# Kernel optimization log

Hardware: AMD Instinct MI355X
Metric: run time of the kernel (lower is better)

The kernel has to match this reference:

```python
import jax, jax.numpy as jnp
import numpy as np

B, T, I, Hd = 64, 512, 256, 512
SIGMA = 0.01


def setup_inputs() -> dict:
    key = jax.random.key(0)
    ks = jax.random.split(key, 32)
    d = {}
    d["tt_inputs"] = jax.random.normal(ks[0], (B, T, I), dtype=jnp.float32)
    d["mark_inputs"] = jax.random.normal(ks[1], (B, T, I), dtype=jnp.float32)
    i = 2
    for nm in ["W_xz_t", "W_xr_t", "W_xz_m", "W_xr_m", "W_xh"]:
        d[nm] = SIGMA * jax.random.normal(ks[i], (I, Hd), dtype=jnp.float32); i += 1
    for nm in ["W_hz_t", "W_hr_t", "W_hz_m", "W_hr_m", "W_hh"]:
        d[nm] = SIGMA * jax.random.normal(ks[i], (Hd, Hd), dtype=jnp.float32); i += 1
    for nm in ["b_z_t", "b_r_t", "b_z_m", "b_r_m", "b_h"]:
        d[nm] = jnp.zeros((Hd,), dtype=jnp.float32)
    for nm in ["fus_W_rt", "fus_W_rm", "fus_W_zt", "fus_W_zm"]:
        d[nm] = jax.random.uniform(ks[i], (Hd, Hd), minval=-0.1, maxval=0.1, dtype=jnp.float32); i += 1
    for nm in ["fus_W_xt", "fus_W_xm"]:
        d[nm] = jax.random.uniform(ks[i], (I, I), minval=-0.1, maxval=0.1, dtype=jnp.float32); i += 1
    for nm, dim in [("fus_rbias", Hd), ("fus_zbias", Hd), ("fus_xbias", I)]:
        d[nm] = jax.random.uniform(ks[i], (dim,), minval=-0.1, maxval=0.1, dtype=jnp.float32); i += 1
    return d


def reference(tt_inputs, mark_inputs,
              W_xz_t, W_xr_t, W_xz_m, W_xr_m, W_xh,
              W_hz_t, W_hr_t, W_hz_m, W_hr_m, W_hh,
              b_z_t, b_r_t, b_z_m, b_r_m, b_h,
              fus_W_rt, fus_W_rm, fus_W_zt, fus_W_zm,
              fus_W_xt, fus_W_xm,
              fus_rbias, fus_zbias, fus_xbias):
    sig = jax.nn.sigmoid
    H0 = jnp.zeros((tt_inputs.shape[0], W_hh.shape[0]), dtype=tt_inputs.dtype)

    def step(H, xs):
        X_t, X_m = xs  # each [B, I]
        Z_t = sig(X_t @ W_xz_t + H @ W_hz_t + b_z_t)
        R_t = sig(X_t @ W_xr_t + H @ W_hr_t + b_r_t)
        Z_m = sig(X_m @ W_xz_m + H @ W_hz_m + b_z_m)
        R_m = sig(X_m @ W_xr_m + H @ W_hr_m + b_r_m)
        z = sig(Z_t @ fus_W_zt + Z_m @ fus_W_zm + fus_zbias)
        Z = z * Z_t + (1 - z) * Z_m
        r = sig(R_t @ fus_W_rt + R_m @ fus_W_rm + fus_rbias)
        R = r * R_t + (1 - r) * R_m
        x = sig(X_t @ fus_W_xt + X_m @ fus_W_xm + fus_xbias)
        X = x * X_t + (1 - x) * X_m
        H_tilde = jnp.tanh(X @ W_xh + (R * H) @ W_hh + b_h)
        H_new = Z * H + (1 - Z) * H_tilde
        return H_new, H_new

    xs = (jnp.swapaxes(tt_inputs, 0, 1), jnp.swapaxes(mark_inputs, 0, 1))  # [T,B,I]
    H_last, outs = jax.lax.scan(step, H0, xs)
    outputs = jnp.swapaxes(outs, 0, 1)  # [B, T, Hd]; dropout p=0.0 -> identity
    return outputs, H_last
```

## Files before the change

kernel.cpp:

```cpp
#include <hip/hip_runtime.h>

#define DEV __device__ __forceinline__

constexpr int Bb = 64, Tt = 512, Ii = 256, Hd = 512;
constexpr int NWG = 512, NTHR = 256;
constexpr int BbHd = Bb * Hd, BbIi = Bb * Ii;


constexpr int OFF_G  = 16384;
constexpr int OFF_F  = OFF_G + 4 * BbHd;
constexpr int OFF_HB = OFF_F + 2 * BbHd;
constexpr int OFF_XB = OFF_HB + 2 * BbHd;
constexpr int OFF_AH = OFF_XB + 2 * BbIi;

#define SMEM_BYTES 32768

struct P {
  const float *tt, *mark;
  const float *Wxz_t, *Wxr_t, *Wxz_m, *Wxr_m, *Wxh;
  const float *Whz_t, *Whr_t, *Whz_m, *Whr_m, *Whh;
  const float *bz_t, *br_t, *bz_m, *br_m, *bh;
  const float *fWrt, *fWrm, *fWzt, *fWzm, *fWxt, *fWxm;
  const float *frb, *fzb, *fxb;
  float* out; float* ws;
};

enum { JA = 0, JB = 1, JRH = 2, JX = 3, JXB = 4 };

DEV float sig1(float x) { return 1.f / (1.f + __expf(-x)); }
DEV float tanh1(float x) { return 2.f * sig1(2.f * x) - 1.f; }
DEV float4 ld4(const float* p) { return *(const float4*)p; }

DEV float2 ld2v(const float* p) {
  unsigned long long u = __hip_atomic_load((const unsigned long long*)p,
                                           __ATOMIC_RELAXED, __HIP_MEMORY_SCOPE_AGENT);
  return __builtin_bit_cast(float2, u);
}
DEV void st2v(float* p, float2 v) {
  __hip_atomic_store((unsigned long long*)p, __builtin_bit_cast(unsigned long long, v),
                     __ATOMIC_RELAXED, __HIP_MEMORY_SCOPE_AGENT);
}
DEV float4 ld4v(const float* p) {
  float2 a = ld2v(p), b = ld2v(p + 2);
  return make_float4(a.x, a.y, b.x, b.y);
}

template<int TYPE>
DEV float4 loadA4(const P& p, int t, const float* aux, int side, int b, int k) {
  const float* ws = p.ws;
  if constexpr (TYPE == JA) {
    if (k < Ii) return ld4(&aux[(b * Tt + (t - 1)) * Ii + k]);
    return ld4v(ws + OFF_HB + ((t - 1) & 1) * BbHd + b * Hd + (k - Ii));
  } else if constexpr (TYPE == JB) {
    const int g = (k < Hd) ? side : side + 2;
    const int j = (k < Hd) ? k : k - Hd;
    return ld4v(ws + OFF_G + g * BbHd + b * Hd + j);
  } else if constexpr (TYPE == JRH) {
    return ld4v(ws + OFF_F + BbHd + b * Hd + k);
  } else if constexpr (TYPE == JX) {
    if (k < Ii) return ld4(&p.tt[(b * Tt + t) * Ii + k]);
    return ld4(&p.mark[(b * Tt + t) * Ii + (k - Ii)]);
  } else {
    return ld4v(ws + OFF_XB + ((t + 1) & 1) * BbIi + b * Ii + k);
  }
}

template<int TYPE, int K, int KSPL, int NC, int CPT>
DEV float2 job8(const P& p, float* lds, int t, const float* aux, int side, int rb,
                int n0, const float* wA, int sA, const float* wB, int sB) {
  const int tid = threadIdx.x;
  constexpr int Kq = K / 4;
  for (int idx = tid; idx < 8 * Kq; idx += NTHR) {
    const int r = idx / Kq, i4 = (idx - r * Kq) * 4;
    float4 v = loadA4<TYPE>(p, t, aux, side, rb + r, i4);
    *(float4*)&lds[r * K + i4] = v;
  }
  __syncthreads();
  constexpr int TPS = NC / CPT;
  constexpr int S = NTHR / TPS;
  constexpr int Kper = K / S;
  const int kk = tid / TPS, cq = tid % TPS;
  const int c0 = n0 + CPT * cq;
  const int kbase = kk * Kper;
  float acc[8][CPT] = {};
  #pragma unroll 2
  for (int i = 0; i < Kper / 2; ++i) {
    const int k = kbase + 2 * i;
    const float* wr0 = (k < KSPL) ? &wA[k * sA] : &wB[(k - KSPL) * sB];
    const float* wr1 = (k + 1 < KSPL) ? &wA[(k + 1) * sA] : &wB[(k + 1 - KSPL) * sB];
    float w0[CPT], w1[CPT];
    if constexpr (CPT == 4) {
      float4 u0 = ld4(&wr0[c0]); w0[0]=u0.x; w0[1]=u0.y; w0[2]=u0.z; w0[3]=u0.w;
      float4 u1 = ld4(&wr1[c0]); w1[0]=u1.x; w1[1]=u1.y; w1[2]=u1.z; w1[3]=u1.w;
    } else {
      float2 u0 = *(const float2*)&wr0[c0]; w0[0]=u0.x; w0[1]=u0.y;
      float2 u1 = *(const float2*)&wr1[c0]; w1[0]=u1.x; w1[1]=u1.y;
    }
    #pragma unroll
    for (int r = 0; r < 8; ++r) {
      float2 a = *(const float2*)&lds[r * K + k];
      #pragma unroll
      for (int c = 0; c < CPT; ++c)
        acc[r][c] = fmaf(a.y, w1[c], fmaf(a.x, w0[c], acc[r][c]));
    }
  }
  __syncthreads();
  float* red = lds;
  #pragma unroll
  for (int r = 0; r < 8; ++r) {
    if constexpr (CPT == 4) {
      *(float4*)&red[(kk * 8 + r) * NC + CPT * cq] =
          make_float4(acc[r][0], acc[r][1], acc[r][2], acc[r][3]);
    } else {
      *(float2*)&red[(kk * 8 + r) * NC + CPT * cq] = make_float2(acc[r][0], acc[r][1]);
    }
  }
  __syncthreads();
  float2 s = make_float2(0.f, 0.f);
  const int e = tid * 2;
  if (e < 8 * NC) {
    #pragma unroll
    for (int q = 0; q < S; ++q) {
      float2 v = *(const float2*)&red[q * 8 * NC + e];
      s.x += v.x; s.y += v.y;
    }
  }
  return s;
}

DEV void grpbar(float* ws, int g, unsigned tgt) {
  __syncthreads();
  if (threadIdx.x == 0) {
    asm volatile("s_waitcnt vmcnt(0)" ::: "memory");
    unsigned* cnt = (unsigned*)ws + g * 64;
    unsigned* gen = (unsigned*)ws + g * 64 + 32;
    unsigned a = __hip_atomic_fetch_add(cnt, 1u, __ATOMIC_RELAXED, __HIP_MEMORY_SCOPE_AGENT);
    if (a == 64u * tgt - 1u)
      __hip_atomic_store(gen, tgt, __ATOMIC_RELAXED, __HIP_MEMORY_SCOPE_AGENT);
    while (__hip_atomic_load(gen, __ATOMIC_RELAXED, __HIP_MEMORY_SCOPE_AGENT) < tgt)
      __builtin_amdgcn_s_sleep(1);
  }
  __syncthreads();
}

__global__ void ggru_init(float* ws) {
  const int i = blockIdx.x * 256 + threadIdx.x;
  if (i < 16384) ws[i] = 0.f;
  const int j = i - 16384;
  if (j >= 0 && j < BbHd) ws[OFF_HB + j] = 0.f;
}

__global__ __launch_bounds__(NTHR)
void ggru_persist(P p) {
  extern __shared__ float sm[];
  const int wg = blockIdx.x, tid = threadIdx.x;
  const int g = wg >> 6, j = wg & 63, rb = g * 8;
  float* ws = p.ws;
  unsigned bt = 0;
  const int e = tid * 2;

  if (j < 16) {
    float2 s = job8<JX, 512, 256, 16, 2>(p, sm, 0, nullptr, 0, rb, j * 16, p.fWxt, Ii, p.fWxm, Ii);
    if (tid < 64) {
      const int r = e >> 4, c = e & 15, col = j * 16 + c, brow = rb + r;
      float2 bv = *(const float2*)&p.fxb[col];
      float g0 = sig1(s.x + bv.x), g1 = sig1(s.y + bv.y);
      float2 xt = *(const float2*)&p.tt[(brow * Tt + 0) * Ii + col];
      float2 xm = *(const float2*)&p.mark[(brow * Tt + 0) * Ii + col];
      st2v(ws + OFF_XB + 1 * BbIi + brow * Ii + col,
           make_float2(g0 * xt.x + (1.f - g0) * xm.x, g1 * xt.y + (1.f - g1) * xm.y));
    }
  }
  grpbar(ws, g, ++bt);
  if (j < 16) {
    float2 s = job8<JXB, 256, 256, 32, 4>(p, sm, 0, nullptr, 0, rb, j * 32, p.Wxh, Hd, p.Wxh, Hd);
    if (tid < 128) {
      const int r = e >> 5, c = e & 31, col = j * 32 + c;
      st2v(ws + OFF_AH + 1 * BbHd + (rb + r) * Hd + col, s);
    }
  }
  grpbar(ws, g, ++bt);

  for (int t = 1; t <= Tt; ++t) {
    {
      const int gate = j >> 4, cb = j & 15, n0 = cb * 32;
      const float* wx = gate==0 ? p.Wxz_t : gate==1 ? p.Wxr_t : gate==2 ? p.Wxz_m : p.Wxr_m;
      const float* wh = gate==0 ? p.Whz_t : gate==1 ? p.Whr_t : gate==2 ? p.Whz_m : p.Whr_m;
      const float* xin = (gate < 2) ? p.tt : p.mark;
      float2 s = job8<JA, 768, 256, 32, 4>(p, sm, t, xin, 0, rb, n0, wx, Hd, wh, Hd);
      if (tid < 128) {
        const int r = e >> 5, c = e & 31, col = n0 + c;
        const float* bias = gate==0 ? p.bz_t : gate==1 ? p.br_t : gate==2 ? p.bz_m : p.br_m;
        float2 bv = *(const float2*)&bias[col];
        st2v(ws + OFF_G + gate * BbHd + (rb + r) * Hd + col,
             make_float2(sig1(s.x + bv.x), sig1(s.y + bv.y)));
      }
    }
    grpbar(ws, g, ++bt);
    if (j < 32) {
      const int side = j >> 4, n0 = (j & 15) * 32;
      const float* wa = side ? p.fWrt : p.fWzt;
      const float* wb = side ? p.fWrm : p.fWzm;
      float2 s = job8<JB, 1024, 512, 32, 4>(p, sm, t, nullptr, side, rb, n0, wa, Hd, wb, Hd);
      if (tid < 128) {
        const int r = e >> 5, c = e & 31, col = n0 + c;
        const int base = (rb + r) * Hd + col;
        const float* bias = side ? p.frb : p.fzb;
        float2 bv = *(const float2*)&bias[col];
        float2 gg = make_float2(sig1(s.x + bv.x), sig1(s.y + bv.y));
        if (side == 0) {
          st2v(ws + OFF_F + base, gg);
        } else {
          float2 rt = ld2v(ws + OFF_G + 1 * BbHd + base);
          float2 rm = ld2v(ws + OFF_G + 3 * BbHd + base);
          float2 ho = ld2v(ws + OFF_HB + ((t - 1) & 1) * BbHd + base);
          st2v(ws + OFF_F + BbHd + base,
               make_float2((gg.x * rt.x + (1.f - gg.x) * rm.x) * ho.x,
                           (gg.y * rt.y + (1.f - gg.y) * rm.y) * ho.y));
        }
      }
    } else if (j < 48 && t < Tt) {
      const int jj = j - 32, n0 = jj * 16;
      float2 s = job8<JX, 512, 256, 16, 2>(p, sm, t, nullptr, 0, rb, n0, p.fWxt, Ii, p.fWxm, Ii);
      if (tid < 64) {
        const int r = e >> 4, c = e & 15, col = n0 + c, brow = rb + r;
        float2 bv = *(const float2*)&p.fxb[col];
        float g0 = sig1(s.x + bv.x), g1 = sig1(s.y + bv.y);
        float2 xt = *(const float2*)&p.tt[(brow * Tt + t) * Ii + col];
        float2 xm = *(const float2*)&p.mark[(brow * Tt + t) * Ii + col];
        st2v(ws + OFF_XB + ((t + 1) & 1) * BbIi + brow * Ii + col,
             make_float2(g0 * xt.x + (1.f - g0) * xm.x, g1 * xt.y + (1.f - g1) * xm.y));
      }
    }
    grpbar(ws, g, ++bt);
    if (j < 32) {
      const int n0 = j * 16;
      float2 s = job8<JRH, 512, 512, 16, 2>(p, sm, t, nullptr, 0, rb, n0, p.Whh, Hd, p.Whh, Hd);
      if (tid < 64) {
        const int r = e >> 4, c = e & 15, col = n0 + c, brow = rb + r;
        const int base = brow * Hd + col;
        float2 ah = ld2v(ws + OFF_AH + (t & 1) * BbHd + base);
        float2 bv = *(const float2*)&p.bh[col];
        float ht0 = tanh1(s.x + ah.x + bv.x), ht1 = tanh1(s.y + ah.y + bv.y);
        float2 zf = ld2v(ws + OFF_F + base);
        float2 zt = ld2v(ws + OFF_G + base);
        float2 zm = ld2v(ws + OFF_G + 2 * BbHd + base);
        float2 ho = ld2v(ws + OFF_HB + ((t - 1) & 1) * BbHd + base);
        float Z0 = zf.x * zt.x + (1.f - zf.x) * zm.x;
        float Z1 = zf.y * zt.y + (1.f - zf.y) * zm.y;
        float2 hn = make_float2(Z0 * ho.x + (1.f - Z0) * ht0, Z1 * ho.y + (1.f - Z1) * ht1);
        st2v(ws + OFF_HB + (t & 1) * BbHd + base, hn);
        *(float2*)&p.out[(brow * Tt + (t - 1)) * Hd + col] = hn;
        if (t == Tt) *(float2*)&p.out[Bb * Tt * Hd + brow * Hd + col] = hn;
      }
    } else if (j < 48 && t < Tt) {
      const int jj = j - 32, n0 = jj * 32;
      float2 s = job8<JXB, 256, 256, 32, 4>(p, sm, t, nullptr, 0, rb, n0, p.Wxh, Hd, p.Wxh, Hd);
      if (tid < 128) {
        const int r = e >> 5, c = e & 31, col = n0 + c;
        st2v(ws + OFF_AH + ((t + 1) & 1) * BbHd + (rb + r) * Hd + col, s);
      }
    }
    grpbar(ws, g, ++bt);
  }
}

extern "C" void kernel_launch(void* const* d_in, const int* in_sizes, int n_in,
                              void* d_out, int out_size, void* d_ws, size_t ws_size,
                              hipStream_t stream) {
  P pr;
  pr.tt    = (const float*)d_in[0];
  pr.mark  = (const float*)d_in[1];
  pr.Wxz_t = (const float*)d_in[2];
  pr.Wxr_t = (const float*)d_in[3];
  pr.Wxz_m = (const float*)d_in[4];
  pr.Wxr_m = (const float*)d_in[5];
  pr.Wxh   = (const float*)d_in[6];
  pr.Whz_t = (const float*)d_in[7];
  pr.Whr_t = (const float*)d_in[8];
  pr.Whz_m = (const float*)d_in[9];
  pr.Whr_m = (const float*)d_in[10];
  pr.Whh   = (const float*)d_in[11];
  pr.bz_t  = (const float*)d_in[12];
  pr.br_t  = (const float*)d_in[13];
  pr.bz_m  = (const float*)d_in[14];
  pr.br_m  = (const float*)d_in[15];
  pr.bh    = (const float*)d_in[16];
  pr.fWrt  = (const float*)d_in[17];
  pr.fWrm  = (const float*)d_in[18];
  pr.fWzt  = (const float*)d_in[19];
  pr.fWzm  = (const float*)d_in[20];
  pr.fWxt  = (const float*)d_in[21];
  pr.fWxm  = (const float*)d_in[22];
  pr.frb   = (const float*)d_in[23];
  pr.fzb   = (const float*)d_in[24];
  pr.fxb   = (const float*)d_in[25];
  pr.out = (float*)d_out;
  pr.ws  = (float*)d_ws;

  hipLaunchKernelGGL(ggru_init, dim3(192), dim3(256), 0, stream, (float*)d_ws);

  void* args[] = { (void*)&pr };
  hipError_t err = hipLaunchCooperativeKernel((const void*)ggru_persist,
                                              dim3(NWG), dim3(NTHR),
                                              args, (unsigned)SMEM_BYTES, stream);
  if (err != hipSuccess) {
    hipLaunchKernelGGL(ggru_persist, dim3(NWG), dim3(NTHR), SMEM_BYTES, stream, pr);
  }
}
```

Before: 11.60 ms.

## Double persistent workgroups by splitting each batch group into 4-row halves

Doubles the persistent grid from 512 to 1024 workgroups, with each workgroup computing 4 batch rows instead of 8. The goal is to spread each recurrent step's matmul work across more CUs so each phase between barriers is shorter. The cost is that every weight tile is now streamed twice per step (once per row half), and each group barrier must wait for 128 arrivals instead of 64. It also depends on 1024 workgroups being co-resident, or the spin barrier could deadlock.

```diff
diff --git a/kernel.cpp b/kernel.cpp
--- a/kernel.cpp
+++ b/kernel.cpp
@@ -3,7 +3,7 @@
 #define DEV __device__ __forceinline__
 
 constexpr int Bb = 64, Tt = 512, Ii = 256, Hd = 512;
-constexpr int NWG = 512, NTHR = 256;
+constexpr int NWG = 1024, NTHR = 256;
 constexpr int BbHd = Bb * Hd, BbIi = Bb * Ii;
 
 
@@ -13,7 +13,7 @@
 constexpr int OFF_XB = OFF_HB + 2 * BbHd;
 constexpr int OFF_AH = OFF_XB + 2 * BbIi;
 
-#define SMEM_BYTES 32768
+#define SMEM_BYTES 16384
 
 struct P {
   const float *tt, *mark;
@@ -66,13 +66,13 @@
 }
 
 template<int TYPE, int K, int KSPL, int NC, int CPT>
-DEV float2 job8(const P& p, float* lds, int t, const float* aux, int side, int rb,
+DEV float2 job4(const P& p, float* lds, int t, const float* aux, int side, int rbj,
                 int n0, const float* wA, int sA, const float* wB, int sB) {
   const int tid = threadIdx.x;
   constexpr int Kq = K / 4;
-  for (int idx = tid; idx < 8 * Kq; idx += NTHR) {
+  for (int idx = tid; idx < 4 * Kq; idx += NTHR) {
     const int r = idx / Kq, i4 = (idx - r * Kq) * 4;
-    float4 v = loadA4<TYPE>(p, t, aux, side, rb + r, i4);
+    float4 v = loadA4<TYPE>(p, t, aux, side, rbj + r, i4);
     *(float4*)&lds[r * K + i4] = v;
   }
   __syncthreads();
@@ -82,7 +82,7 @@
   const int kk = tid / TPS, cq = tid % TPS;
   const int c0 = n0 + CPT * cq;
   const int kbase = kk * Kper;
-  float acc[8][CPT] = {};
+  float acc[4][CPT] = {};
   #pragma unroll 2
   for (int i = 0; i < Kper / 2; ++i) {
     const int k = kbase + 2 * i;
@@ -97,7 +97,7 @@
       float2 u1 = *(const float2*)&wr1[c0]; w1[0]=u1.x; w1[1]=u1.y;
     }
     #pragma unroll
-    for (int r = 0; r < 8; ++r) {
+    for (int r = 0; r < 4; ++r) {
       float2 a = *(const float2*)&lds[r * K + k];
       #pragma unroll
       for (int c = 0; c < CPT; ++c)
@@ -107,21 +107,21 @@
   __syncthreads();
   float* red = lds;
   #pragma unroll
-  for (int r = 0; r < 8; ++r) {
+  for (int r = 0; r < 4; ++r) {
     if constexpr (CPT == 4) {
-      *(float4*)&red[(kk * 8 + r) * NC + CPT * cq] =
+      *(float4*)&red[(kk * 4 + r) * NC + CPT * cq] =
           make_float4(acc[r][0], acc[r][1], acc[r][2], acc[r][3]);
     } else {
-      *(float2*)&red[(kk * 8 + r) * NC + CPT * cq] = make_float2(acc[r][0], acc[r][1]);
+      *(float2*)&red[(kk * 4 + r) * NC + CPT * cq] = make_float2(acc[r][0], acc[r][1]);
     }
   }
   __syncthreads();
   float2 s = make_float2(0.f, 0.f);
   const int e = tid * 2;
-  if (e < 8 * NC) {
+  if (e < 4 * NC) {
     #pragma unroll
     for (int q = 0; q < S; ++q) {
-      float2 v = *(const float2*)&red[q * 8 * NC + e];
+      float2 v = *(const float2*)&red[q * 4 * NC + e];
       s.x += v.x; s.y += v.y;
     }
   }
@@ -135,7 +135,7 @@
     unsigned* cnt = (unsigned*)ws + g * 64;
     unsigned* gen = (unsigned*)ws + g * 64 + 32;
     unsigned a = __hip_atomic_fetch_add(cnt, 1u, __ATOMIC_RELAXED, __HIP_MEMORY_SCOPE_AGENT);
-    if (a == 64u * tgt - 1u)
+    if (a == 128u * tgt - 1u)
       __hip_atomic_store(gen, tgt, __ATOMIC_RELAXED, __HIP_MEMORY_SCOPE_AGENT);
     while (__hip_atomic_load(gen, __ATOMIC_RELAXED, __HIP_MEMORY_SCOPE_AGENT) < tgt)
       __builtin_amdgcn_s_sleep(1);
@@ -154,15 +154,16 @@
 void ggru_persist(P p) {
   extern __shared__ float sm[];
   const int wg = blockIdx.x, tid = threadIdx.x;
-  const int g = wg >> 6, j = wg & 63, rb = g * 8;
+  const int g = wg >> 7, j = wg & 127, rb = g * 8;
   float* ws = p.ws;
   unsigned bt = 0;
   const int e = tid * 2;
 
-  if (j < 16) {
-    float2 s = job8<JX, 512, 256, 16, 2>(p, sm, 0, nullptr, 0, rb, j * 16, p.fWxt, Ii, p.fWxm, Ii);
-    if (tid < 64) {
-      const int r = e >> 4, c = e & 15, col = j * 16 + c, brow = rb + r;
+  if (j < 32) {
+    const int rh = j >> 4, cb = j & 15, n0 = cb * 16, rbj = rb + rh * 4;
+    float2 s = job4<JX, 512, 256, 16, 2>(p, sm, 0, nullptr, 0, rbj, n0, p.fWxt, Ii, p.fWxm, Ii);
+    if (e < 64) {
+      const int r = e >> 4, c = e & 15, col = n0 + c, brow = rbj + r;
       float2 bv = *(const float2*)&p.fxb[col];
       float g0 = sig1(s.x + bv.x), g1 = sig1(s.y + bv.y);
       float2 xt = *(const float2*)&p.tt[(brow * Tt + 0) * Ii + col];
@@ -172,39 +173,42 @@
     }
   }
   grpbar(ws, g, ++bt);
-  if (j < 16) {
-    float2 s = job8<JXB, 256, 256, 32, 4>(p, sm, 0, nullptr, 0, rb, j * 32, p.Wxh, Hd, p.Wxh, Hd);
-    if (tid < 128) {
-      const int r = e >> 5, c = e & 31, col = j * 32 + c;
-      st2v(ws + OFF_AH + 1 * BbHd + (rb + r) * Hd + col, s);
+  if (j < 64) {
+    const int rh = j >> 5, cb = j & 31, n0 = cb * 16, rbj = rb + rh * 4;
+    float2 s = job4<JXB, 256, 256, 16, 2>(p, sm, 0, nullptr, 0, rbj, n0, p.Wxh, Hd, p.Wxh, Hd);
+    if (e < 64) {
+      const int r = e >> 4, c = e & 15, col = n0 + c;
+      st2v(ws + OFF_AH + 1 * BbHd + (rbj + r) * Hd + col, s);
     }
   }
   grpbar(ws, g, ++bt);
 
   for (int t = 1; t <= Tt; ++t) {
     {
-      const int gate = j >> 4, cb = j & 15, n0 = cb * 32;
+      const int gate = j >> 5, rh = (j >> 4) & 1, cb = j & 15, n0 = cb * 32;
+      const int rbj = rb + rh * 4;
       const float* wx = gate==0 ? p.Wxz_t : gate==1 ? p.Wxr_t : gate==2 ? p.Wxz_m : p.Wxr_m;
       const float* wh = gate==0 ? p.Whz_t : gate==1 ? p.Whr_t : gate==2 ? p.Whz_m : p.Whr_m;
       const float* xin = (gate < 2) ? p.tt : p.mark;
-      float2 s = job8<JA, 768, 256, 32, 4>(p, sm, t, xin, 0, rb, n0, wx, Hd, wh, Hd);
-      if (tid < 128) {
+      float2 s = job4<JA, 768, 256, 32, 4>(p, sm, t, xin, 0, rbj, n0, wx, Hd, wh, Hd);
+      if (e < 128) {
         const int r = e >> 5, c = e & 31, col = n0 + c;
         const float* bias = gate==0 ? p.bz_t : gate==1 ? p.br_t : gate==2 ? p.bz_m : p.br_m;
         float2 bv = *(const float2*)&bias[col];
-        st2v(ws + OFF_G + gate * BbHd + (rb + r) * Hd + col,
+        st2v(ws + OFF_G + gate * BbHd + (rbj + r) * Hd + col,
              make_float2(sig1(s.x + bv.x), sig1(s.y + bv.y)));
       }
     }
     grpbar(ws, g, ++bt);
-    if (j < 32) {
-      const int side = j >> 4, n0 = (j & 15) * 32;
+    if (j < 64) {
+      const int side = j >> 5, rh = (j >> 4) & 1, cb = j & 15, n0 = cb * 32;
+      const int rbj = rb + rh * 4;
       const float* wa = side ? p.fWrt : p.fWzt;
       const float* wb = side ? p.fWrm : p.fWzm;
-      float2 s = job8<JB, 1024, 512, 32, 4>(p, sm, t, nullptr, side, rb, n0, wa, Hd, wb, Hd);
-      if (tid < 128) {
+      float2 s = job4<JB, 1024, 512, 32, 4>(p, sm, t, nullptr, side, rbj, n0, wa, Hd, wb, Hd);
+      if (e < 128) {
         const int r = e >> 5, c = e & 31, col = n0 + c;
-        const int base = (rb + r) * Hd + col;
+        const int base = (rbj + r) * Hd + col;
         const float* bias = side ? p.frb : p.fzb;
         float2 bv = *(const float2*)&bias[col];
         float2 gg = make_float2(sig1(s.x + bv.x), sig1(s.y + bv.y));
@@ -219,11 +223,12 @@
                            (gg.y * rt.y + (1.f - gg.y) * rm.y) * ho.y));
         }
       }
-    } else if (j < 48 && t < Tt) {
-      const int jj = j - 32, n0 = jj * 16;
-      float2 s = job8<JX, 512, 256, 16, 2>(p, sm, t, nullptr, 0, rb, n0, p.fWxt, Ii, p.fWxm, Ii);
-      if (tid < 64) {
-        const int r = e >> 4, c = e & 15, col = n0 + c, brow = rb + r;
+    } else if (j < 96 && t < Tt) {
+      const int jj = j - 64, rh = jj >> 4, cb = jj & 15, n0 = cb * 16;
+      const int rbj = rb + rh * 4;
+      float2 s = job4<JX, 512, 256, 16, 2>(p, sm, t, nullptr, 0, rbj, n0, p.fWxt, Ii, p.fWxm, Ii);
+      if (e < 64) {
+        const int r = e >> 4, c = e & 15, col = n0 + c, brow = rbj + r;
         float2 bv = *(const float2*)&p.fxb[col];
         float g0 = sig1(s.x + bv.x), g1 = sig1(s.y + bv.y);
         float2 xt = *(const float2*)&p.tt[(brow * Tt + t) * Ii + col];
@@ -233,11 +238,11 @@
       }
     }
     grpbar(ws, g, ++bt);
-    if (j < 32) {
-      const int n0 = j * 16;
-      float2 s = job8<JRH, 512, 512, 16, 2>(p, sm, t, nullptr, 0, rb, n0, p.Whh, Hd, p.Whh, Hd);
-      if (tid < 64) {
-        const int r = e >> 4, c = e & 15, col = n0 + c, brow = rb + r;
+    if (j < 64) {
+      const int rh = j >> 5, cb = j & 31, n0 = cb * 16, rbj = rb + rh * 4;
+      float2 s = job4<JRH, 512, 512, 16, 2>(p, sm, t, nullptr, 0, rbj, n0, p.Whh, Hd, p.Whh, Hd);
+      if (e < 64) {
+        const int r = e >> 4, c = e & 15, col = n0 + c, brow = rbj + r;
         const int base = brow * Hd + col;
         float2 ah = ld2v(ws + OFF_AH + (t & 1) * BbHd + base);
         float2 bv = *(const float2*)&p.bh[col];
@@ -253,12 +258,13 @@
         *(float2*)&p.out[(brow * Tt + (t - 1)) * Hd + col] = hn;
         if (t == Tt) *(float2*)&p.out[Bb * Tt * Hd + brow * Hd + col] = hn;
       }
-    } else if (j < 48 && t < Tt) {
-      const int jj = j - 32, n0 = jj * 32;
-      float2 s = job8<JXB, 256, 256, 32, 4>(p, sm, t, nullptr, 0, rb, n0, p.Wxh, Hd, p.Wxh, Hd);
-      if (tid < 128) {
-        const int r = e >> 5, c = e & 31, col = n0 + c;
-        st2v(ws + OFF_AH + ((t + 1) & 1) * BbHd + (rb + r) * Hd + col, s);
+    } else if (t < Tt) {
+      const int jj = j - 64, rh = jj >> 5, cb = jj & 31, n0 = cb * 16;
+      const int rbj = rb + rh * 4;
+      float2 s = job4<JXB, 256, 256, 16, 2>(p, sm, t, nullptr, 0, rbj, n0, p.Wxh, Hd, p.Wxh, Hd);
+      if (e < 64) {
+        const int r = e >> 4, c = e & 15, col = n0 + c;
+        st2v(ws + OFF_AH + ((t + 1) & 1) * BbHd + (rbj + r) * Hd + col, s);
       }
     }
     grpbar(ws, g, ++bt);
```

Measured after the change: 17.34 ms. +49.4%, slower.

## Precompute input-gate projections a step ahead and rebalance phase work across groups

Applied to the files above, without the earlier changes.

The X@W_x{z,r} input projections for the four gates move out of the recurrent gate phase into a new workspace buffer (OFF_XA), computed one timestep ahead during the last phase by otherwise idle workgroups. The recurrent gate GEMM then only reduces over H (K=512 instead of 768). The fusion-gate phase now spreads across all 64 workgroups in the group, and the X-fusion work is shifted two steps ahead into the final phase. The aim is to shorten the serial critical path per timestep, at the cost of more workspace and a more complex schedule across phases.

```diff
diff --git a/kernel.cpp b/kernel.cpp
--- a/kernel.cpp
+++ b/kernel.cpp
@@ -5,6 +5,7 @@
 constexpr int Bb = 64, Tt = 512, Ii = 256, Hd = 512;
 constexpr int NWG = 512, NTHR = 256;
 constexpr int BbHd = Bb * Hd, BbIi = Bb * Ii;
+constexpr int BbXA = Bb * 2048;
 
 
 constexpr int OFF_G  = 16384;
@@ -12,6 +13,7 @@
 constexpr int OFF_HB = OFF_F + 2 * BbHd;
 constexpr int OFF_XB = OFF_HB + 2 * BbHd;
 constexpr int OFF_AH = OFF_XB + 2 * BbIi;
+constexpr int OFF_XA = OFF_AH + 2 * BbHd;
 
 #define SMEM_BYTES 32768
 
@@ -25,7 +27,7 @@
   float* out; float* ws;
 };
 
-enum { JA = 0, JB = 1, JRH = 2, JX = 3, JXB = 4 };
+enum { JA = 0, JB = 1, JRH = 2, JX = 3, JXB = 4, JX2 = 5 };
 
 DEV float sig1(float x) { return 1.f / (1.f + __expf(-x)); }
 DEV float tanh1(float x) { return 2.f * sig1(2.f * x) - 1.f; }
@@ -49,8 +51,7 @@
 DEV float4 loadA4(const P& p, int t, const float* aux, int side, int b, int k) {
   const float* ws = p.ws;
   if constexpr (TYPE == JA) {
-    if (k < Ii) return ld4(&aux[(b * Tt + (t - 1)) * Ii + k]);
-    return ld4v(ws + OFF_HB + ((t - 1) & 1) * BbHd + b * Hd + (k - Ii));
+    return ld4v(ws + OFF_HB + ((t - 1) & 1) * BbHd + b * Hd + k);
   } else if constexpr (TYPE == JB) {
     const int g = (k < Hd) ? side : side + 2;
     const int j = (k < Hd) ? k : k - Hd;
@@ -60,8 +61,10 @@
   } else if constexpr (TYPE == JX) {
     if (k < Ii) return ld4(&p.tt[(b * Tt + t) * Ii + k]);
     return ld4(&p.mark[(b * Tt + t) * Ii + (k - Ii)]);
+  } else if constexpr (TYPE == JXB) {
+    return ld4v(ws + OFF_XB + ((t + 1) & 1) * BbIi + b * Ii + k);
   } else {
-    return ld4v(ws + OFF_XB + ((t + 1) & 1) * BbIi + b * Ii + k);
+    return ld4(&aux[(b * Tt + t) * Ii + k]);
   }
 }
 
@@ -159,51 +162,58 @@
   unsigned bt = 0;
   const int e = tid * 2;
 
-  if (j < 16) {
-    float2 s = job8<JX, 512, 256, 16, 2>(p, sm, 0, nullptr, 0, rb, j * 16, p.fWxt, Ii, p.fWxm, Ii);
-    if (tid < 64) {
-      const int r = e >> 4, c = e & 15, col = j * 16 + c, brow = rb + r;
+  if (j < 32) {
+    const int gate = j >> 3, cb = j & 7, n0 = cb * 64;
+    const float* wx = gate==0 ? p.Wxz_t : gate==1 ? p.Wxr_t : gate==2 ? p.Wxz_m : p.Wxr_m;
+    const float* xin = (gate < 2) ? p.tt : p.mark;
+    float2 s = job8<JX2, 256, 256, 64, 4>(p, sm, 0, xin, 0, rb, n0, wx, Hd, wx, Hd);
+    const int r = e >> 6, c = e & 63, col = n0 + c;
+    st2v(ws + OFF_XA + 1 * BbXA + (rb + r) * 2048 + gate * 512 + col, s);
+  } else if (j < 48) {
+    const int inst = (j - 32) >> 3, jj = (j - 32) & 7, n0 = jj * 32;
+    const int tp = inst;
+    float2 s = job8<JX, 512, 256, 32, 4>(p, sm, tp, nullptr, 0, rb, n0, p.fWxt, Ii, p.fWxm, Ii);
+    if (tid < 128) {
+      const int r = e >> 5, c = e & 31, col = n0 + c, brow = rb + r;
       float2 bv = *(const float2*)&p.fxb[col];
       float g0 = sig1(s.x + bv.x), g1 = sig1(s.y + bv.y);
-      float2 xt = *(const float2*)&p.tt[(brow * Tt + 0) * Ii + col];
-      float2 xm = *(const float2*)&p.mark[(brow * Tt + 0) * Ii + col];
-      st2v(ws + OFF_XB + 1 * BbIi + brow * Ii + col,
+      float2 xt = *(const float2*)&p.tt[(brow * Tt + tp) * Ii + col];
+      float2 xm = *(const float2*)&p.mark[(brow * Tt + tp) * Ii + col];
+      st2v(ws + OFF_XB + ((tp + 1) & 1) * BbIi + brow * Ii + col,
            make_float2(g0 * xt.x + (1.f - g0) * xm.x, g1 * xt.y + (1.f - g1) * xm.y));
     }
   }
   grpbar(ws, g, ++bt);
-  if (j < 16) {
-    float2 s = job8<JXB, 256, 256, 32, 4>(p, sm, 0, nullptr, 0, rb, j * 32, p.Wxh, Hd, p.Wxh, Hd);
-    if (tid < 128) {
-      const int r = e >> 5, c = e & 31, col = j * 32 + c;
-      st2v(ws + OFF_AH + 1 * BbHd + (rb + r) * Hd + col, s);
-    }
+  if (j < 8) {
+    const int n0 = j * 64;
+    float2 s = job8<JXB, 256, 256, 64, 4>(p, sm, 0, nullptr, 0, rb, n0, p.Wxh, Hd, p.Wxh, Hd);
+    const int r = e >> 6, c = e & 63, col = n0 + c;
+    st2v(ws + OFF_AH + 1 * BbHd + (rb + r) * Hd + col, s);
   }
   grpbar(ws, g, ++bt);
 
   for (int t = 1; t <= Tt; ++t) {
     {
       const int gate = j >> 4, cb = j & 15, n0 = cb * 32;
-      const float* wx = gate==0 ? p.Wxz_t : gate==1 ? p.Wxr_t : gate==2 ? p.Wxz_m : p.Wxr_m;
       const float* wh = gate==0 ? p.Whz_t : gate==1 ? p.Whr_t : gate==2 ? p.Whz_m : p.Whr_m;
-      const float* xin = (gate < 2) ? p.tt : p.mark;
-      float2 s = job8<JA, 768, 256, 32, 4>(p, sm, t, xin, 0, rb, n0, wx, Hd, wh, Hd);
+      float2 s = job8<JA, 512, 512, 32, 4>(p, sm, t, nullptr, 0, rb, n0, wh, Hd, wh, Hd);
       if (tid < 128) {
         const int r = e >> 5, c = e & 31, col = n0 + c;
+        float2 xa = ld2v(ws + OFF_XA + (t & 1) * BbXA + (rb + r) * 2048 + gate * 512 + col);
         const float* bias = gate==0 ? p.bz_t : gate==1 ? p.br_t : gate==2 ? p.bz_m : p.br_m;
         float2 bv = *(const float2*)&bias[col];
         st2v(ws + OFF_G + gate * BbHd + (rb + r) * Hd + col,
-             make_float2(sig1(s.x + bv.x), sig1(s.y + bv.y)));
+             make_float2(sig1(s.x + xa.x + bv.x), sig1(s.y + xa.y + bv.y)));
       }
     }
     grpbar(ws, g, ++bt);
-    if (j < 32) {
-      const int side = j >> 4, n0 = (j & 15) * 32;
+    {
+      const int side = j >> 5, n0 = (j & 31) * 16;
       const float* wa = side ? p.fWrt : p.fWzt;
       const float* wb = side ? p.fWrm : p.fWzm;
-      float2 s = job8<JB, 1024, 512, 32, 4>(p, sm, t, nullptr, side, rb, n0, wa, Hd, wb, Hd);
-      if (tid < 128) {
-        const int r = e >> 5, c = e & 31, col = n0 + c;
+      float2 s = job8<JB, 1024, 512, 16, 2>(p, sm, t, nullptr, side, rb, n0, wa, Hd, wb, Hd);
+      if (tid < 64) {
+        const int r = e >> 4, c = e & 15, col = n0 + c;
         const int base = (rb + r) * Hd + col;
         const float* bias = side ? p.frb : p.fzb;
         float2 bv = *(const float2*)&bias[col];
@@ -219,25 +229,22 @@
                            (gg.y * rt.y + (1.f - gg.y) * rm.y) * ho.y));
         }
       }
-    } else if (j < 48 && t < Tt) {
-      const int jj = j - 32, n0 = jj * 16;
-      float2 s = job8<JX, 512, 256, 16, 2>(p, sm, t, nullptr, 0, rb, n0, p.fWxt, Ii, p.fWxm, Ii);
-      if (tid < 64) {
-        const int r = e >> 4, c = e & 15, col = n0 + c, brow = rb + r;
-        float2 bv = *(const float2*)&p.fxb[col];
-        float g0 = sig1(s.x + bv.x), g1 = sig1(s.y + bv.y);
-        float2 xt = *(const float2*)&p.tt[(brow * Tt + t) * Ii + col];
-        float2 xm = *(const float2*)&p.mark[(brow * Tt + t) * Ii + col];
-        st2v(ws + OFF_XB + ((t + 1) & 1) * BbIi + brow * Ii + col,
-             make_float2(g0 * xt.x + (1.f - g0) * xm.x, g1 * xt.y + (1.f - g1) * xm.y));
-      }
     }
     grpbar(ws, g, ++bt);
     if (j < 32) {
-      const int n0 = j * 16;
-      float2 s = job8<JRH, 512, 512, 16, 2>(p, sm, t, nullptr, 0, rb, n0, p.Whh, Hd, p.Whh, Hd);
-      if (tid < 64) {
-        const int r = e >> 4, c = e & 15, col = n0 + c, brow = rb + r;
+      if (t < Tt) {
+        const int gate = j >> 3, cb = j & 7, n0 = cb * 64;
+        const float* wx = gate==0 ? p.Wxz_t : gate==1 ? p.Wxr_t : gate==2 ? p.Wxz_m : p.Wxr_m;
+        const float* xin = (gate < 2) ? p.tt : p.mark;
+        float2 s = job8<JX2, 256, 256, 64, 4>(p, sm, t, xin, 0, rb, n0, wx, Hd, wx, Hd);
+        const int r = e >> 6, c = e & 63, col = n0 + c;
+        st2v(ws + OFF_XA + ((t + 1) & 1) * BbXA + (rb + r) * 2048 + gate * 512 + col, s);
+      }
+    } else if (j < 48) {
+      const int jj = j - 32, n0 = jj * 32;
+      float2 s = job8<JRH, 512, 512, 32, 4>(p, sm, t, nullptr, 0, rb, n0, p.Whh, Hd, p.Whh, Hd);
+      if (tid < 128) {
+        const int r = e >> 5, c = e & 31, col = n0 + c, brow = rb + r;
         const int base = brow * Hd + col;
         float2 ah = ld2v(ws + OFF_AH + (t & 1) * BbHd + base);
         float2 bv = *(const float2*)&p.bh[col];
@@ -253,12 +260,27 @@
         *(float2*)&p.out[(brow * Tt + (t - 1)) * Hd + col] = hn;
         if (t == Tt) *(float2*)&p.out[Bb * Tt * Hd + brow * Hd + col] = hn;
       }
-    } else if (j < 48 && t < Tt) {
-      const int jj = j - 32, n0 = jj * 32;
-      float2 s = job8<JXB, 256, 256, 32, 4>(p, sm, t, nullptr, 0, rb, n0, p.Wxh, Hd, p.Wxh, Hd);
-      if (tid < 128) {
-        const int r = e >> 5, c = e & 31, col = n0 + c;
+    } else if (j < 56) {
+      if (t < Tt) {
+        const int jj = j - 48, n0 = jj * 64;
+        float2 s = job8<JXB, 256, 256, 64, 4>(p, sm, t, nullptr, 0, rb, n0, p.Wxh, Hd, p.Wxh, Hd);
+        const int r = e >> 6, c = e & 63, col = n0 + c;
         st2v(ws + OFF_AH + ((t + 1) & 1) * BbHd + (rb + r) * Hd + col, s);
+      }
+    } else {
+      if (t + 1 < Tt) {
+        const int jj = j - 56, n0 = jj * 32;
+        const int tp = t + 1;
+        float2 s = job8<JX, 512, 256, 32, 4>(p, sm, tp, nullptr, 0, rb, n0, p.fWxt, Ii, p.fWxm, Ii);
+        if (tid < 128) {
+          const int r = e >> 5, c = e & 31, col = n0 + c, brow = rb + r;
+          float2 bv = *(const float2*)&p.fxb[col];
+          float g0 = sig1(s.x + bv.x), g1 = sig1(s.y + bv.y);
+          float2 xt = *(const float2*)&p.tt[(brow * Tt + tp) * Ii + col];
+          float2 xm = *(const float2*)&p.mark[(brow * Tt + tp) * Ii + col];
+          st2v(ws + OFF_XB + ((tp + 1) & 1) * BbIi + brow * Ii + col,
+               make_float2(g0 * xt.x + (1.f - g0) * xm.x, g1 * xt.y + (1.f - g1) * xm.y));
+        }
       }
     }
     grpbar(ws, g, ++bt);
```

Result: faster. 10.68 ms (-7.9%).
